# Optimization experiments

Measured on AMD Instinct MI355X. Metric: run time of the kernel, lower is better.

Reference implementation:

```python
import jax, jax.numpy as jnp
import numpy as np

B, N, NFG, NFR = 512, 64, 1024, 256
OH, OW = 87, 157
POS_THRESHOLD = 0.2


def setup_inputs() -> dict:
    key = jax.random.key(0)
    ks = jax.random.split(key, 7)
    feats = jax.random.normal(ks[0], (B, N, NFG), dtype=jnp.float32)
    # boxes (x1,y1,x2,y2) in image coordinates
    boxes = jax.random.uniform(ks[1], (B, N, 4), dtype=jnp.float32)
    scale = jnp.array([OW, OH, OW, OH], dtype=jnp.float32)
    boxes = boxes * scale
    s_in = 1.0 / np.sqrt(NFG)
    W_theta = jax.random.normal(ks[2], (NFG, NFR), dtype=jnp.float32) * s_in
    b_theta = jnp.zeros((NFR,), dtype=jnp.float32)
    W_phi = jax.random.normal(ks[3], (NFG, NFR), dtype=jnp.float32) * s_in
    b_phi = jnp.zeros((NFR,), dtype=jnp.float32)
    W_gcn = jax.random.normal(ks[4], (NFG, NFG), dtype=jnp.float32) * s_in
    return {
        "graph_boxes_features": feats,
        "boxes_in_flat": boxes,
        "W_theta": W_theta,
        "b_theta": b_theta,
        "W_phi": W_phi,
        "b_phi": b_phi,
        "W_gcn": W_gcn,
    }


def reference(graph_boxes_features, boxes_in_flat, W_theta, b_theta, W_phi, b_phi, W_gcn):
    nfr = W_theta.shape[-1]
    # box centers [B,N,2]
    cx = (boxes_in_flat[..., 0] + boxes_in_flat[..., 2]) * 0.5
    cy = (boxes_in_flat[..., 1] + boxes_in_flat[..., 3]) * 0.5
    pos = jnp.stack([cx, cy], axis=-1)  # [B,N,2]
    # pairwise euclidean distances [B,N,N]
    diff = pos[:, :, None, :] - pos[:, None, :, :]
    dist = jnp.sqrt(jnp.sum(diff * diff, axis=-1))
    position_mask = dist > (POS_THRESHOLD * OW)

    theta = jnp.einsum('bnf,fr->bnr', graph_boxes_features, W_theta) + b_theta
    phi = jnp.einsum('bnf,fr->bnr', graph_boxes_features, W_phi) + b_phi
    sim = jnp.einsum('bnr,bmr->bnm', theta, phi) / jnp.sqrt(jnp.asarray(nfr, theta.dtype))
    logits = jnp.where(position_mask, -jnp.inf, sim)
    relation_graph = jax.nn.softmax(logits, axis=2)  # [B,N,N]

    agg = jnp.einsum('bnm,bmf->bnf', relation_graph, graph_boxes_features)
    out = jax.nn.relu(jnp.einsum('bnf,fg->bng', agg, W_gcn))
    return out, relation_graph
```

## Files before the change

kernel.cpp:

```cpp
#include <hip/hip_runtime.h>
#include <hip/hip_bf16.h>
#include <math.h>

#define BB   512
#define NN   64
#define NFG  1024
#define NFR  256
#define MM   (BB * NN)
#define RG_OFF 33554432L

typedef __attribute__((ext_vector_type(8))) short bf16x8;
typedef __attribute__((ext_vector_type(4))) float f32x4;
typedef __attribute__((ext_vector_type(8))) unsigned short u16x8;

__device__ inline unsigned short f2bf(float f) {
    union { float f; unsigned u; } v; v.f = f;
    unsigned u = v.u;
    return (unsigned short)((u + 0x7FFFu + ((u >> 16) & 1u)) >> 16);
}

__device__ inline void gld_lds16(const unsigned short* g, unsigned short* l) {
    __builtin_amdgcn_global_load_lds((const __attribute__((address_space(1))) void*)g,
                                     (__attribute__((address_space(3))) void*)l, 16, 0, 0);
}


__global__ __launch_bounds__(256) void cast_f32_bf16(const float* __restrict__ in,
                                                     unsigned short* __restrict__ out, long n) {
    long i = ((long)blockIdx.x * 256 + threadIdx.x) * 8;
    if (i + 8 <= n) {
        f32x4 a = *(const f32x4*)(in + i);
        f32x4 b = *(const f32x4*)(in + i + 4);
        u16x8 o;
#pragma unroll
        for (int c = 0; c < 4; ++c) { o[c] = f2bf(a[c]); o[4 + c] = f2bf(b[c]); }
        *(u16x8*)(out + i) = o;
    }
}

__global__ void transpose_cast(const float* __restrict__ in, unsigned short* __restrict__ out,
                               int K, int N) {
    __shared__ float tile[32][33];
    int tx = threadIdx.x, ty = threadIdx.y;
    int k0 = blockIdx.y * 32, n0 = blockIdx.x * 32;
#pragma unroll
    for (int r = 0; r < 4; ++r)
        tile[ty + r * 8][tx] = in[(long)(k0 + ty + r * 8) * N + n0 + tx];
    __syncthreads();
#pragma unroll
    for (int r = 0; r < 4; ++r)
        out[(long)(n0 + ty + r * 8) * K + k0 + tx] = f2bf(tile[tx][ty + r * 8]);
}

__global__ void concat_bias(const float* __restrict__ bt, const float* __restrict__ bp,
                            float* __restrict__ out) {
    int i = threadIdx.x;
    out[i] = (i < 256) ? bt[i] : bp[i - 256];
}


template<int RELU, int STORE_BF16, int SWIZ, int LOG_FAST>
__global__ __launch_bounds__(256, 4)
void gemm_bt(const unsigned short* __restrict__ A, const unsigned short* __restrict__ Bt,
             const float* __restrict__ bias, void* __restrict__ Cout,
             int M, int N, int K) {
    __shared__ __align__(16) unsigned short As[128 * 64];
    __shared__ __align__(16) unsigned short Bs[128 * 64];
    const int t    = threadIdx.x;
    const int lane = t & 63;
    const int w    = t >> 6;
    const int l15  = lane & 15;
    const int q    = lane >> 4;

    long mtile, ntile;
    if (SWIZ == 1) {
        long linear = (long)blockIdx.y * gridDim.x + blockIdx.x;
        int  xcd  = (int)(linear & 7);
        long slot = linear >> 3;
        mtile = slot & ((1 << LOG_FAST) - 1);
        ntile = (long)xcd * (gridDim.y >> 3) + (slot >> LOG_FAST);
    } else if (SWIZ == 2) {
        long linear = (long)blockIdx.y * gridDim.x + blockIdx.x;
        int  xcd  = (int)(linear & 7);
        long slot = linear >> 3;
        ntile = slot & ((1 << LOG_FAST) - 1);
        mtile = (long)xcd * (gridDim.x >> 3) + (slot >> LOG_FAST);
    } else {
        mtile = blockIdx.x; ntile = blockIdx.y;
    }
    const long tileM = mtile * 128;
    const long tileN = ntile * 128;
    const int wm = (w & 1) * 64;
    const int wn = (w >> 1) * 64;

    f32x4 acc[4][4] = {};

    const int rS = t >> 3;
    const int cS = (t & 7) ^ (rS & 7);
    const unsigned short* gA = A  + (tileM + rS) * (long)K + cS * 8;
    const unsigned short* gB = Bt + (tileN + rS) * (long)K + cS * 8;

    for (int kt = 0; kt < K; kt += 64) {
        __syncthreads();
#pragma unroll
        for (int i = 0; i < 4; ++i) {
            gld_lds16(gA + (long)i * 32 * K + kt, As + (i * 256 + w * 64) * 8);
            gld_lds16(gB + (long)i * 32 * K + kt, Bs + (i * 256 + w * 64) * 8);
        }
        __syncthreads();
#pragma unroll
        for (int ks = 0; ks < 2; ++ks) {
            const int slot = (ks * 4 + q) ^ (l15 & 7);
            bf16x8 af[4], bf[4];
#pragma unroll
            for (int mi = 0; mi < 4; ++mi)
                af[mi] = *(const bf16x8*)(As + (wm + mi * 16 + l15) * 64 + slot * 8);
#pragma unroll
            for (int ni = 0; ni < 4; ++ni)
                bf[ni] = *(const bf16x8*)(Bs + (wn + ni * 16 + l15) * 64 + slot * 8);
#pragma unroll
            for (int mi = 0; mi < 4; ++mi)
#pragma unroll
                for (int ni = 0; ni < 4; ++ni)
                    acc[mi][ni] = __builtin_amdgcn_mfma_f32_16x16x32_bf16(af[mi], bf[ni],
                                                                          acc[mi][ni], 0, 0, 0);
        }
    }

#pragma unroll
    for (int mi = 0; mi < 4; ++mi) {
#pragma unroll
        for (int ni = 0; ni < 4; ++ni) {
            long row0 = tileM + wm + mi * 16 + q * 4;
            long col  = tileN + wn + ni * 16 + l15;
            float bv = bias ? bias[col] : 0.f;
#pragma unroll
            for (int r = 0; r < 4; ++r) {
                float v = acc[mi][ni][r] + bv;
                if (RELU) v = fmaxf(v, 0.f);
                long idx = (row0 + r) * N + col;
                if (STORE_BF16) ((unsigned short*)Cout)[idx] = f2bf(v);
                else            ((float*)Cout)[idx] = v;
            }
        }
    }
}


__global__ __launch_bounds__(256)
void fused_softmax_out(const unsigned short* __restrict__ thetaphi,
                       const float* __restrict__ boxes,
                       const unsigned short* __restrict__ HtT,
                       float* __restrict__ rg_out,
                       float* __restrict__ out) {
    __shared__ __align__(16) float sim_s[64][68];
    __shared__ __align__(16) unsigned short Pb[64][72];
    __shared__ float cxs[64], cys[64];
    const int t    = threadIdx.x;
    const int b    = blockIdx.x;
    const int lane = t & 63;
    const int w    = t >> 6;
    const int l15  = lane & 15;
    const int q    = lane >> 4;

    if (t < 64) {
        float4 bx = *(const float4*)(boxes + ((long)b * 64 + t) * 4);
        cxs[t] = (bx.x + bx.z) * 0.5f;
        cys[t] = (bx.y + bx.w) * 0.5f;
    }

    {
        f32x4 acc[4] = {};
        const unsigned short* thA = thetaphi + ((long)b * 64 + w * 16 + l15) * 512 + q * 8;
        const unsigned short* thB = thetaphi + ((long)b * 64 + l15) * 512 + 256 + q * 8;
#pragma unroll
        for (int kt = 0; kt < 256; kt += 32) {
            bf16x8 a = *(const bf16x8*)(thA + kt);
#pragma unroll
            for (int ni = 0; ni < 4; ++ni) {
                bf16x8 bb = *(const bf16x8*)(thB + (long)ni * 16 * 512 + kt);
                acc[ni] = __builtin_amdgcn_mfma_f32_16x16x32_bf16(a, bb, acc[ni], 0, 0, 0);
            }
        }
#pragma unroll
        for (int ni = 0; ni < 4; ++ni)
#pragma unroll
            for (int r = 0; r < 4; ++r)
                sim_s[w * 16 + q * 4 + r][ni * 16 + l15] = acc[ni][r] * 0.0625f;
    }
    __syncthreads();

    {
        const int i  = t >> 2;
        const int j0 = (t & 3) * 16;
        const float cxi = cxs[i], cyi = cys[i];
        const float thr = (float)(0.2 * 157.0);
        float vals[16];
        float mx = -__builtin_inff();
#pragma unroll
        for (int jj = 0; jj < 16; ++jj) {
            int j = j0 + jj;
            float dx = cxi - cxs[j];
            float dy = cyi - cys[j];
            bool msk = sqrtf(dx * dx + dy * dy) > thr;
            float s = msk ? -__builtin_inff() : sim_s[i][j];
            vals[jj] = s;
            mx = fmaxf(mx, s);
        }
        mx = fmaxf(mx, __shfl_xor(mx, 1, 64));
        mx = fmaxf(mx, __shfl_xor(mx, 2, 64));
        float sum = 0.f;
#pragma unroll
        for (int jj = 0; jj < 16; ++jj) {
            float e = (vals[jj] == -__builtin_inff()) ? 0.f : __expf(vals[jj] - mx);
            vals[jj] = e;
            sum += e;
        }
        sum += __shfl_xor(sum, 1, 64);
        sum += __shfl_xor(sum, 2, 64);
        float inv = 1.f / sum;
#pragma unroll
        for (int jj = 0; jj < 16; ++jj) {
            int j = j0 + jj;
            float p = vals[jj] * inv;
            rg_out[((long)b * 64 + i) * 64 + j] = p;
            Pb[i][j] = f2bf(p);
        }
    }
    __syncthreads();

    {
        const unsigned short* HtB = HtT + (long)b * 64;
        float* outB = out + (long)b * 65536;
        bf16x8 af[4][2];
#pragma unroll
        for (int mi = 0; mi < 4; ++mi)
#pragma unroll
            for (int kk = 0; kk < 2; ++kk)
                af[mi][kk] = *(const bf16x8*)(&Pb[mi * 16 + l15][kk * 32 + q * 8]);
#pragma unroll 2
        for (int nt = 0; nt < 16; ++nt) {
            const int g0 = w * 256 + nt * 16;
            const unsigned short* hp = HtB + (long)(g0 + l15) * 32768 + q * 8;
            bf16x8 b0 = *(const bf16x8*)(hp);
            bf16x8 b1 = *(const bf16x8*)(hp + 32);
#pragma unroll
            for (int mi = 0; mi < 4; ++mi) {
                f32x4 acc = {};
                acc = __builtin_amdgcn_mfma_f32_16x16x32_bf16(af[mi][0], b0, acc, 0, 0, 0);
                acc = __builtin_amdgcn_mfma_f32_16x16x32_bf16(af[mi][1], b1, acc, 0, 0, 0);
#pragma unroll
                for (int r = 0; r < 4; ++r)
                    outB[(long)(mi * 16 + q * 4 + r) * 1024 + g0 + l15] = fmaxf(acc[r], 0.f);
            }
        }
    }
}


extern "C" void kernel_launch(void* const* d_in, const int* in_sizes, int n_in,
                              void* d_out, int out_size, void* d_ws, size_t ws_size,
                              hipStream_t stream) {
    const float* feats   = (const float*)d_in[0];
    const float* boxes   = (const float*)d_in[1];
    const float* W_theta = (const float*)d_in[2];
    const float* b_theta = (const float*)d_in[3];
    const float* W_phi   = (const float*)d_in[4];
    const float* b_phi   = (const float*)d_in[5];
    const float* W_gcn   = (const float*)d_in[6];
    float* out = (float*)d_out;

    char* ws = (char*)d_ws;
    unsigned short* featsb   = (unsigned short*)(ws);
    unsigned short* thetaphi = (unsigned short*)(ws + 67108864);
    unsigned short* HtT      = (unsigned short*)(ws + 100663296);
    unsigned short* Wtp      = (unsigned short*)(ws + 167772160);
    unsigned short* Wgt      = (unsigned short*)(ws + 168820736);
    float*          bias512  = (float*)(ws + 170917888);

    cast_f32_bf16<<<16384, 256, 0, stream>>>(feats, featsb, 33554432L);
    transpose_cast<<<dim3(8, 32),  dim3(32, 8), 0, stream>>>(W_theta, Wtp,              1024, 256);
    transpose_cast<<<dim3(8, 32),  dim3(32, 8), 0, stream>>>(W_phi,   Wtp + 256 * 1024, 1024, 256);
    transpose_cast<<<dim3(32, 32), dim3(32, 8), 0, stream>>>(W_gcn,   Wgt,              1024, 1024);
    concat_bias<<<1, 512, 0, stream>>>(b_theta, b_phi, bias512);

    gemm_bt<0, 1, 2, 2><<<dim3(256, 4), 256, 0, stream>>>(featsb, Wtp, bias512, thetaphi,
                                                          MM, 512, 1024);
    gemm_bt<0, 1, 1, 3><<<dim3(8, 256), 256, 0, stream>>>(Wgt, featsb, nullptr, HtT,
                                                          1024, MM, 1024);
    fused_softmax_out<<<BB, 256, 0, stream>>>(thetaphi, boxes, HtT, out + RG_OFF, out);
}
```

Measured before the change: 432.7 us.

## Triple-buffer GEMM loads and enlarge tiles to 128x256 with 512 threads

Rewrites the bf16 GEMM kernel to use a three-stage LDS ring buffer. Global-to-LDS loads for k-step j+2 are issued while step j computes, and a vmcnt wait replaces the pair of barriers per iteration. The block tile grows to 128x256 with 8 waves, and MFMA sections get raised wave priority. This targets load latency stalls and barrier overhead. In exchange LDS use rises to 144KB per block, which limits occupancy, and correctness depends on the hand-written vmcnt counts.

```diff
diff --git a/kernel.cpp b/kernel.cpp
--- a/kernel.cpp
+++ b/kernel.cpp
@@ -60,38 +60,37 @@
 
 
 template<int RELU, int STORE_BF16, int SWIZ, int LOG_FAST>
-__global__ __launch_bounds__(256, 4)
-void gemm_bt(const unsigned short* __restrict__ A, const unsigned short* __restrict__ Bt,
-             const float* __restrict__ bias, void* __restrict__ Cout,
-             int M, int N, int K) {
-    __shared__ __align__(16) unsigned short As[128 * 64];
-    __shared__ __align__(16) unsigned short Bs[128 * 64];
+__global__ __launch_bounds__(512, 2)
+void gemm_bt3(const unsigned short* __restrict__ A, const unsigned short* __restrict__ Bt,
+              const float* __restrict__ bias, void* __restrict__ Cout,
+              int M, int N, int K) {
+    __shared__ __align__(16) unsigned short As[3 * 128 * 64];
+    __shared__ __align__(16) unsigned short Bs[3 * 256 * 64];
     const int t    = threadIdx.x;
     const int lane = t & 63;
     const int w    = t >> 6;
     const int l15  = lane & 15;
     const int q    = lane >> 4;
 
+    const int mtiles = M >> 7;
+    const int ntiles = N >> 8;
     long mtile, ntile;
-    if (SWIZ == 1) {
-        long linear = (long)blockIdx.y * gridDim.x + blockIdx.x;
-        int  xcd  = (int)(linear & 7);
-        long slot = linear >> 3;
-        mtile = slot & ((1 << LOG_FAST) - 1);
-        ntile = (long)xcd * (gridDim.y >> 3) + (slot >> LOG_FAST);
-    } else if (SWIZ == 2) {
-        long linear = (long)blockIdx.y * gridDim.x + blockIdx.x;
-        int  xcd  = (int)(linear & 7);
-        long slot = linear >> 3;
-        ntile = slot & ((1 << LOG_FAST) - 1);
-        mtile = (long)xcd * (gridDim.x >> 3) + (slot >> LOG_FAST);
-    } else {
-        mtile = blockIdx.x; ntile = blockIdx.y;
+    {
+        long lin  = blockIdx.x;
+        int  xcd  = (int)(lin & 7);
+        long slot = lin >> 3;
+        if (SWIZ == 2) {
+            ntile = slot & ((1 << LOG_FAST) - 1);
+            mtile = (long)xcd * (mtiles >> 3) + (slot >> LOG_FAST);
+        } else {
+            mtile = slot & ((1 << LOG_FAST) - 1);
+            ntile = (long)xcd * (ntiles >> 3) + (slot >> LOG_FAST);
+        }
     }
     const long tileM = mtile * 128;
-    const long tileN = ntile * 128;
-    const int wm = (w & 1) * 64;
-    const int wn = (w >> 1) * 64;
+    const long tileN = ntile * 256;
+    const int wm = (w >> 2) * 64;
+    const int wn = (w & 3) * 64;
 
     f32x4 acc[4][4] = {};
 
@@ -99,31 +98,47 @@
     const int cS = (t & 7) ^ (rS & 7);
     const unsigned short* gA = A  + (tileM + rS) * (long)K + cS * 8;
     const unsigned short* gB = Bt + (tileN + rS) * (long)K + cS * 8;
-
-    for (int kt = 0; kt < K; kt += 64) {
-        __syncthreads();
-#pragma unroll
-        for (int i = 0; i < 4; ++i) {
-            gld_lds16(gA + (long)i * 32 * K + kt, As + (i * 256 + w * 64) * 8);
-            gld_lds16(gB + (long)i * 32 * K + kt, Bs + (i * 256 + w * 64) * 8);
-        }
-        __syncthreads();
+    const int NTk = K >> 6;
+
+    auto STAGE = [&](int j) {
+        const int  buf = j % 3;
+        const long kt  = (long)j * 64;
+#pragma unroll
+        for (int i = 0; i < 2; ++i)
+            gld_lds16(gA + (long)i * 64 * K + kt, As + buf * 8192  + (i * 512 + w * 64) * 8);
+#pragma unroll
+        for (int i = 0; i < 4; ++i)
+            gld_lds16(gB + (long)i * 64 * K + kt, Bs + buf * 16384 + (i * 512 + w * 64) * 8);
+    };
+
+    STAGE(0);
+    STAGE(1);
+
+    for (int j = 0; j < NTk; ++j) {
+        const int buf = j % 3;
+        if (j < NTk - 1) asm volatile("s_waitcnt vmcnt(6)" ::: "memory");
+        else             asm volatile("s_waitcnt vmcnt(0)" ::: "memory");
+        __builtin_amdgcn_s_barrier();
+        __builtin_amdgcn_sched_barrier(0);
+        if (j + 2 < NTk) STAGE(j + 2);
 #pragma unroll
         for (int ks = 0; ks < 2; ++ks) {
             const int slot = (ks * 4 + q) ^ (l15 & 7);
             bf16x8 af[4], bf[4];
 #pragma unroll
             for (int mi = 0; mi < 4; ++mi)
-                af[mi] = *(const bf16x8*)(As + (wm + mi * 16 + l15) * 64 + slot * 8);
+                af[mi] = *(const bf16x8*)(As + buf * 8192  + (wm + mi * 16 + l15) * 64 + slot * 8);
 #pragma unroll
             for (int ni = 0; ni < 4; ++ni)
-                bf[ni] = *(const bf16x8*)(Bs + (wn + ni * 16 + l15) * 64 + slot * 8);
+                bf[ni] = *(const bf16x8*)(Bs + buf * 16384 + (wn + ni * 16 + l15) * 64 + slot * 8);
+            __builtin_amdgcn_s_setprio(1);
 #pragma unroll
             for (int mi = 0; mi < 4; ++mi)
 #pragma unroll
                 for (int ni = 0; ni < 4; ++ni)
                     acc[mi][ni] = __builtin_amdgcn_mfma_f32_16x16x32_bf16(af[mi], bf[ni],
                                                                           acc[mi][ni], 0, 0, 0);
+            __builtin_amdgcn_s_setprio(0);
         }
     }
 
@@ -284,9 +299,9 @@
     transpose_cast<<<dim3(32, 32), dim3(32, 8), 0, stream>>>(W_gcn,   Wgt,              1024, 1024);
     concat_bias<<<1, 512, 0, stream>>>(b_theta, b_phi, bias512);
 
-    gemm_bt<0, 1, 2, 2><<<dim3(256, 4), 256, 0, stream>>>(featsb, Wtp, bias512, thetaphi,
-                                                          MM, 512, 1024);
-    gemm_bt<0, 1, 1, 3><<<dim3(8, 256), 256, 0, stream>>>(Wgt, featsb, nullptr, HtT,
-                                                          1024, MM, 1024);
+    gemm_bt3<0, 1, 2, 1><<<512, 512, 0, stream>>>(featsb, Wtp, bias512, thetaphi,
+                                                  MM, 512, 1024);
+    gemm_bt3<0, 1, 1, 3><<<1024, 512, 0, stream>>>(Wgt, featsb, nullptr, HtT,
+                                                   1024, MM, 1024);
     fused_softmax_out<<<BB, 256, 0, stream>>>(thetaphi, boxes, HtT, out + RG_OFF, out);
 }
```

New measurement: 482.7 us. 11.6% more time.

## Merge prep kernels into one launch and split softmax-output kernel across two blocks per batch

Applied to the files above, without the earlier changes.

Replaces the five small preprocessing launches (feature cast, three weight transposes, bias concat) with a single kernel that dispatches on block index, removing per-launch overhead. The fused softmax/output kernel now uses two blocks per batch element, each computing half of the 1024 output columns. This doubles the grid for better occupancy on the final stage, at the cost of recomputing the similarity and softmax in both halves. Only the first half writes the relation graph.

```diff
diff --git a/kernel.cpp b/kernel.cpp
--- a/kernel.cpp
+++ b/kernel.cpp
@@ -25,24 +25,11 @@
 }
 
 
-__global__ __launch_bounds__(256) void cast_f32_bf16(const float* __restrict__ in,
-                                                     unsigned short* __restrict__ out, long n) {
-    long i = ((long)blockIdx.x * 256 + threadIdx.x) * 8;
-    if (i + 8 <= n) {
-        f32x4 a = *(const f32x4*)(in + i);
-        f32x4 b = *(const f32x4*)(in + i + 4);
-        u16x8 o;
-#pragma unroll
-        for (int c = 0; c < 4; ++c) { o[c] = f2bf(a[c]); o[4 + c] = f2bf(b[c]); }
-        *(u16x8*)(out + i) = o;
-    }
-}
-
-__global__ void transpose_cast(const float* __restrict__ in, unsigned short* __restrict__ out,
-                               int K, int N) {
-    __shared__ float tile[32][33];
-    int tx = threadIdx.x, ty = threadIdx.y;
-    int k0 = blockIdx.y * 32, n0 = blockIdx.x * 32;
+__device__ void tcast_body(const float* __restrict__ in, unsigned short* __restrict__ out,
+                           int K, int N, int bx, int by, float tile[32][33]) {
+    const int t  = threadIdx.x;
+    const int tx = t & 31, ty = t >> 5;
+    const int k0 = by * 32, n0 = bx * 32;
 #pragma unroll
     for (int r = 0; r < 4; ++r)
         tile[ty + r * 8][tx] = in[(long)(k0 + ty + r * 8) * N + n0 + tx];
@@ -52,10 +39,39 @@
         out[(long)(n0 + ty + r * 8) * K + k0 + tx] = f2bf(tile[tx][ty + r * 8]);
 }
 
-__global__ void concat_bias(const float* __restrict__ bt, const float* __restrict__ bp,
-                            float* __restrict__ out) {
-    int i = threadIdx.x;
-    out[i] = (i < 256) ? bt[i] : bp[i - 256];
+__global__ __launch_bounds__(256)
+void prep(const float* __restrict__ feats, unsigned short* __restrict__ featsb,
+          const float* __restrict__ W_theta, const float* __restrict__ W_phi,
+          const float* __restrict__ W_gcn,
+          unsigned short* __restrict__ Wtp, unsigned short* __restrict__ Wgt,
+          const float* __restrict__ bt, const float* __restrict__ bp,
+          float* __restrict__ bias512) {
+    __shared__ float tile[32][33];
+    const int bid = blockIdx.x;
+    const int t   = threadIdx.x;
+    if (bid < 16384) {
+        long i = ((long)bid * 256 + t) * 8;
+        if (i + 8 <= 33554432L) {
+            f32x4 a = *(const f32x4*)(feats + i);
+            f32x4 b = *(const f32x4*)(feats + i + 4);
+            u16x8 o;
+#pragma unroll
+            for (int c = 0; c < 4; ++c) { o[c] = f2bf(a[c]); o[4 + c] = f2bf(b[c]); }
+            *(u16x8*)(featsb + i) = o;
+        }
+    } else if (bid < 16640) {
+        int r = bid - 16384;
+        tcast_body(W_theta, Wtp, 1024, 256, r & 7, r >> 3, tile);
+    } else if (bid < 16896) {
+        int r = bid - 16640;
+        tcast_body(W_phi, Wtp + 256 * 1024, 1024, 256, r & 7, r >> 3, tile);
+    } else if (bid < 17920) {
+        int r = bid - 16896;
+        tcast_body(W_gcn, Wgt, 1024, 1024, r & 31, r >> 5, tile);
+    } else {
+        bias512[t]       = bt[t];
+        bias512[t + 256] = bp[t];
+    }
 }
 
 
@@ -157,7 +173,8 @@
     __shared__ __align__(16) unsigned short Pb[64][72];
     __shared__ float cxs[64], cys[64];
     const int t    = threadIdx.x;
-    const int b    = blockIdx.x;
+    const int b    = blockIdx.x >> 1;
+    const int gh   = blockIdx.x & 1;
     const int lane = t & 63;
     const int w    = t >> 6;
     const int l15  = lane & 15;
@@ -223,7 +240,7 @@
         for (int jj = 0; jj < 16; ++jj) {
             int j = j0 + jj;
             float p = vals[jj] * inv;
-            rg_out[((long)b * 64 + i) * 64 + j] = p;
+            if (gh == 0) rg_out[((long)b * 64 + i) * 64 + j] = p;
             Pb[i][j] = f2bf(p);
         }
     }
@@ -239,8 +256,8 @@
             for (int kk = 0; kk < 2; ++kk)
                 af[mi][kk] = *(const bf16x8*)(&Pb[mi * 16 + l15][kk * 32 + q * 8]);
 #pragma unroll 2
-        for (int nt = 0; nt < 16; ++nt) {
-            const int g0 = w * 256 + nt * 16;
+        for (int nt = 0; nt < 8; ++nt) {
+            const int g0 = gh * 512 + w * 128 + nt * 16;
             const unsigned short* hp = HtB + (long)(g0 + l15) * 32768 + q * 8;
             bf16x8 b0 = *(const bf16x8*)(hp);
             bf16x8 b1 = *(const bf16x8*)(hp + 32);
@@ -278,15 +295,12 @@
     unsigned short* Wgt      = (unsigned short*)(ws + 168820736);
     float*          bias512  = (float*)(ws + 170917888);
 
-    cast_f32_bf16<<<16384, 256, 0, stream>>>(feats, featsb, 33554432L);
-    transpose_cast<<<dim3(8, 32),  dim3(32, 8), 0, stream>>>(W_theta, Wtp,              1024, 256);
-    transpose_cast<<<dim3(8, 32),  dim3(32, 8), 0, stream>>>(W_phi,   Wtp + 256 * 1024, 1024, 256);
-    transpose_cast<<<dim3(32, 32), dim3(32, 8), 0, stream>>>(W_gcn,   Wgt,              1024, 1024);
-    concat_bias<<<1, 512, 0, stream>>>(b_theta, b_phi, bias512);
+    prep<<<17921, 256, 0, stream>>>(feats, featsb, W_theta, W_phi, W_gcn,
+                                    Wtp, Wgt, b_theta, b_phi, bias512);
 
     gemm_bt<0, 1, 2, 2><<<dim3(256, 4), 256, 0, stream>>>(featsb, Wtp, bias512, thetaphi,
                                                           MM, 512, 1024);
     gemm_bt<0, 1, 1, 3><<<dim3(8, 256), 256, 0, stream>>>(Wgt, featsb, nullptr, HtT,
                                                           1024, MM, 1024);
-    fused_softmax_out<<<BB, 256, 0, stream>>>(thetaphi, boxes, HtT, out + RG_OFF, out);
-}
+    fused_softmax_out<<<BB * 2, 256, 0, stream>>>(thetaphi, boxes, HtT, out + RG_OFF, out);
+}
```

New measurement: 435.3 us. Within noise of the previous version (+0.6%).
